# Kernel optimization log

Hardware: AMD Instinct MI355X
Metric: run time of the kernel (lower is better)

The kernel has to match this reference:

```python
import jax, jax.numpy as jnp
import numpy as np
from jax import lax

NUM_HEADS = 8
EPS = 1e-12  # torch F.normalize default eps


def setup_inputs() -> dict:
    key = jax.random.key(0)
    ks = jax.random.split(key, 7)
    B, C, H, W = 4, 128, 256, 256
    d = C // 2  # per-branch channels = 64
    x = jax.random.normal(ks[0], (B, C, H, W), jnp.float32)
    w_qkv1 = jax.random.normal(ks[1], (3 * d, d), jnp.float32) * 0.05
    w_qkv2 = jax.random.normal(ks[2], (3 * d, d), jnp.float32) * 0.05
    w_dw1 = jax.random.normal(ks[3], (3 * d, 1, 3, 3), jnp.float32) * 0.05
    w_dw2 = jax.random.normal(ks[4], (3 * d, 1, 3, 3), jnp.float32) * 0.05
    w_po1 = jax.random.normal(ks[5], (d, d), jnp.float32) * 0.05
    w_po2 = jax.random.normal(ks[6], (d, d), jnp.float32) * 0.05
    t1 = jnp.ones((NUM_HEADS, 1, 1), jnp.float32)
    t2 = jnp.ones((NUM_HEADS, 1, 1), jnp.float32)
    return {"x": x, "w_qkv1": w_qkv1, "w_qkv2": w_qkv2, "w_dw1": w_dw1,
            "w_dw2": w_dw2, "w_po1": w_po1, "w_po2": w_po2, "t1": t1, "t2": t2}


def _qkv(xb, w1x1, wdw):
    # 1x1 conv (pointwise) then 3x3 depthwise conv, no bias
    y = jnp.einsum('bchw,oc->bohw', xb, w1x1)
    y = lax.conv_general_dilated(
        y, wdw, window_strides=(1, 1), padding='SAME',
        dimension_numbers=('NCHW', 'OIHW', 'NCHW'),
        feature_group_count=y.shape[1])
    return y


def _heads(t, b, h, w):
    # b (head c) h w -> b head c (h*w)
    return t.reshape(b, NUM_HEADS, -1, h * w)


def _l2norm(t):
    n = jnp.sqrt(jnp.sum(t * t, axis=-1, keepdims=True))
    return t / jnp.maximum(n, EPS)


def reference(x, w_qkv1, w_qkv2, w_dw1, w_dw2, w_po1, w_po2, t1, t2):
    b, c, h, w = x.shape
    x1, x2 = jnp.split(x, 2, axis=1)
    q1, k1, v1 = jnp.split(_qkv(x1, w_qkv1, w_dw1), 3, axis=1)
    q2, k2, v2 = jnp.split(_qkv(x2, w_qkv2, w_dw2), 3, axis=1)
    q1, k1, v1 = (_heads(t, b, h, w) for t in (q1, k1, v1))
    q2, k2, v2 = (_heads(t, b, h, w) for t in (q2, k2, v2))
    q1, k1 = _l2norm(q1), _l2norm(k1)
    q2, k2 = _l2norm(q2), _l2norm(k2)
    # channel-wise attention: [b, head, c_h, c_h]
    attn1 = jax.nn.softmax(jnp.einsum('bhcn,bhdn->bhcd', q1, k1) * t1[None], axis=-1)
    attn2 = jax.nn.softmax(jnp.einsum('bhcn,bhdn->bhcd', q2, k2) * t2[None], axis=-1)
    # cross-branch V swap
    out1 = jnp.einsum('bhcd,bhdn->bhcn', attn1, v2).reshape(b, c // 2, h, w)
    out2 = jnp.einsum('bhcd,bhdn->bhcn', attn2, v1).reshape(b, c // 2, h, w)
    out1 = jnp.einsum('bchw,oc->bohw', out1, w_po1)
    out2 = jnp.einsum('bchw,oc->bohw', out2, w_po2)
    return jnp.concatenate([out1, out2], axis=1)
```

## Files before the change

kernel.cpp:

```cpp
#include <hip/hip_runtime.h>
#include <hip/hip_fp16.h>

#define NPIX 65536
#define WIMG 256
#define HIMG 256
#define TW 16
#define TH 8
#define HSTR 24
#define NSLOT 240
#define YCH 248

typedef __attribute__((ext_vector_type(8))) _Float16 half8;
typedef __attribute__((ext_vector_type(4))) float f32x4;

__device__ __forceinline__ unsigned int h2u(__half2 h) {
  union { __half2 h; unsigned int u; } c; c.h = h; return c.u;
}
__device__ __forceinline__ __half2 u2h(unsigned int u) {
  union { unsigned int u; __half2 h; } c; c.u = u; return c.h;
}
__device__ __forceinline__ __half2 sp2(_Float16 s) {
  union { _Float16 h[2]; __half2 v; } u; u.h[0] = s; u.h[1] = s; return u.v;
}
__device__ __forceinline__ int qk_idx(int ch, int pxblk) {
  return ch * 128 + ((pxblk ^ (ch & 7)) << 3);
}
__device__ __forceinline__ void ld16_lds(const void* g, void* l) {
  __builtin_amdgcn_global_load_lds(
      (const __attribute__((address_space(1))) unsigned int*)g,
      (__attribute__((address_space(3))) unsigned int*)l, 16, 0, 0);
}

__global__ void k_zero(float* __restrict__ p, int n) {
  int i = blockIdx.x * 256 + threadIdx.x;
  if (i < n) p[i] = 0.0f;
}

__global__ __launch_bounds__(256)
void k_wprep(const float* __restrict__ wq1, const float* __restrict__ wq2,
             const float* __restrict__ wd1, const float* __restrict__ wd2,
             _Float16* __restrict__ wqh, _Float16* __restrict__ wdh) {
  int i = blockIdx.x * 256 + threadIdx.x;
  if (i < 24576) {
    int br = i / 12288, j = i - br * 12288;
    wqh[i] = (_Float16)((br ? wq2 : wq1)[j]);
  } else if (i < 24576 + 6144) {
    int j = i - 24576;
    int br = j / 3072, r = j - br * 3072;
    int o = r >> 4, t = r & 15;
    wdh[j] = (t < 9) ? (_Float16)((br ? wd2 : wd1)[o * 9 + t]) : (_Float16)0.0f;
  }
}

__global__ __launch_bounds__(256)
void k_xt(const float* __restrict__ x, __half* __restrict__ xT) {
  __shared__ _Float16 tile[64 * 257];
  const int strip = blockIdx.x;
  const int br = blockIdx.y, b = blockIdx.z;
  const int tid = threadIdx.x;
  const float* xb = x + ((size_t)b * 128 + br * 64) * NPIX + strip * 256;
  #pragma unroll 8
  for (int c = 0; c < 64; ++c)
    tile[c * 257 + tid] = (_Float16)xb[(size_t)c * NPIX + tid];
  __syncthreads();
  __half* xo = xT + ((size_t)(b * 2 + br) * NPIX + strip * 256) * 64;
  const int j = tid & 7;
  #pragma unroll
  for (int i = 0; i < 8; ++i) {
    int p = (tid >> 3) + i * 32;
    half8 h;
    #pragma unroll
    for (int k = 0; k < 8; ++k) h[k] = tile[(j * 8 + k) * 257 + p];
    *(half8*)((_Float16*)xo + p * 64 + j * 8) = h;
  }
}

__global__ __launch_bounds__(256, 3)
void k_qkv(const __half* __restrict__ xT,
           const _Float16* __restrict__ wqh, const _Float16* __restrict__ wdh,
           const float* __restrict__ zpage,
           __half* __restrict__ vbuf, float* __restrict__ gram,
           float* __restrict__ sqq, float* __restrict__ sqk)
{
  __shared__ __align__(16) _Float16 xs[256 * 64];
  __shared__ __align__(16) _Float16 ys[2 * 16 * YCH];

  const int tid = threadIdx.x;
  const int lane = tid & 63;
  const int wid = tid >> 6;
  const int tile = blockIdx.x;
  const int br = blockIdx.y;
  const int b = blockIdx.z;
  const int tx0 = (tile & 15) * TW;
  const int ty0 = (tile >> 4) * TH;

  const _Float16* wqb = wqh + br * 12288;
  const _Float16* wdb = wdh + br * 3072;
  const __half* xTimg = xT + (size_t)(b * 2 + br) * NPIX * 64;

  {
    const int j = lane & 7, pl = lane >> 3;
    for (int it = wid; it < 30; it += 4) {
      int s = it * 8;
      int slot = s + pl;
      int hy = slot / HSTR;
      int hx = slot - hy * HSTR;
      int gy = ty0 - 1 + hy, gx = tx0 - 1 + hx;
      bool valid = (hx < 18) && ((unsigned)gy < HIMG) && ((unsigned)gx < WIMG);
      const void* src = valid
        ? (const void*)((const _Float16*)xTimg + (size_t)(gy * WIMG + gx) * 64
                        + ((j ^ (slot & 7)) << 3))
        : (const void*)((const char*)zpage + lane * 16);
      ld16_lds(src, (void*)(xs + s * 64));
    }
  }
  asm volatile("s_waitcnt vmcnt(0)" ::: "memory");
  __syncthreads();

  const int col = lane & 15;
  const int qrow = lane >> 4;
  const int rel = wid * 4 + (lane >> 4);
  const int row = (lane >> 1) & 7;
  const int half = lane & 1;

  unsigned int qreg[4][4], kreg[4][4];

#define PW16(S) do {                                                          \
    const int p_ = (S) >> 2, hh_ = (S) & 3;                                   \
    _Float16* yb_ = ys + ((S) & 1) * (16 * YCH);                              \
    const _Float16* wp_ = wqb + (((p_ * 64 + hh_ * 16 + col) << 6) + qrow * 8); \
    half8 wf0_ = *(const half8*)(wp_);                                        \
    half8 wf1_ = *(const half8*)(wp_ + 32);                                   \
    for (int mt = wid; mt < 15; mt += 4) {                                    \
      int px = mt * 16 + col;                                                 \
      half8 af0 = *(const half8*)(xs + px * 64 + (((qrow    ) ^ (px & 7)) << 3)); \
      half8 af1 = *(const half8*)(xs + px * 64 + (((4 + qrow) ^ (px & 7)) << 3)); \
      f32x4 a0 = {0,0,0,0};                                                   \
      a0 = __builtin_amdgcn_mfma_f32_16x16x32_f16(af0, wf0_, a0, 0, 0, 0);    \
      a0 = __builtin_amdgcn_mfma_f32_16x16x32_f16(af1, wf1_, a0, 0, 0, 0);    \
      int pxd = mt * 16 + qrow * 4;                                           \
      uint2 s0_ = {h2u(__floats2half2_rn(a0[0], a0[1])),                      \
                   h2u(__floats2half2_rn(a0[2], a0[3]))};                     \
      *(uint2*)(yb_ + col * YCH + pxd) = s0_;                                 \
    }                                                                         \
  } while (0)

#define DW16(S) do {                                                          \
    const int p_ = (S) >> 2, hh_ = (S) & 3;                                   \
    const _Float16* yb_ = ys + ((S) & 1) * (16 * YCH);                        \
    const int o_ = hh_ * 16 + rel;                                            \
    const _Float16* wdp_ = wdb + ((p_ * 64 + o_) << 4);                       \
    half8 wv_ = *(const half8*)wdp_;                                          \
    _Float16 w8_ = wdp_[8];                                                   \
    __half2 w2_[9];                                                           \
    _Pragma("unroll")                                                         \
    for (int j = 0; j < 8; ++j) w2_[j] = sp2(wv_[j]);                         \
    w2_[8] = sp2(w8_);                                                        \
    __half2 a_[4];                                                            \
    _Pragma("unroll")                                                         \
    for (int k2 = 0; k2 < 4; ++k2) a_[k2] = u2h(0u);                          \
    _Pragma("unroll")                                                         \
    for (int ky = 0; ky < 3; ++ky) {                                          \
      const _Float16* rp_ = yb_ + rel * YCH + (row + ky) * HSTR + half * 8;   \
      uint2 ra_ = *(const uint2*)rp_;                                         \
      uint2 rb_ = *(const uint2*)(rp_ + 4);                                   \
      unsigned int rc_ = *(const unsigned int*)(rp_ + 8);                     \
      unsigned int W_[5] = {ra_.x, ra_.y, rb_.x, rb_.y, rc_};                 \
      _Pragma("unroll")                                                       \
      for (int k2 = 0; k2 < 4; ++k2) {                                        \
        unsigned int M_ = (W_[k2] >> 16) | (W_[k2 + 1] << 16);                \
        a_[k2] = __hfma2(w2_[ky * 3 + 0], u2h(W_[k2]), a_[k2]);               \
        a_[k2] = __hfma2(w2_[ky * 3 + 1], u2h(M_), a_[k2]);                   \
        a_[k2] = __hfma2(w2_[ky * 3 + 2], u2h(W_[k2 + 1]), a_[k2]);           \
      }                                                                       \
    }                                                                         \
    if (p_ == 0) {                                                            \
      _Pragma("unroll")                                                       \
      for (int k2 = 0; k2 < 4; ++k2) qreg[hh_][k2] = h2u(a_[k2]);             \
    } else if (p_ == 1) {                                                     \
      _Pragma("unroll")                                                       \
      for (int k2 = 0; k2 < 4; ++k2) kreg[hh_][k2] = h2u(a_[k2]);             \
    } else {                                                                  \
      __half* vrow_ = (__half*)(vbuf                                          \
          + ((size_t)((br * 4 + b) * 64 + o_)) * NPIX                         \
          + (ty0 + row) * WIMG + tx0 + half * 8);                             \
      uint4 s_ = {h2u(a_[0]), h2u(a_[1]), h2u(a_[2]), h2u(a_[3])};            \
      *(uint4*)vrow_ = s_;                                                    \
    }                                                                         \
  } while (0)

  PW16(0);  __syncthreads();
  PW16(1);  DW16(0);  __syncthreads();
  PW16(2);  DW16(1);  __syncthreads();
  PW16(3);  DW16(2);  __syncthreads();
  PW16(4);  DW16(3);  __syncthreads();
  PW16(5);  DW16(4);  __syncthreads();
  PW16(6);  DW16(5);  __syncthreads();
  PW16(7);  DW16(6);  __syncthreads();
  PW16(8);  DW16(7);  __syncthreads();
  PW16(9);  DW16(8);  __syncthreads();
  PW16(10); DW16(9);  __syncthreads();
  PW16(11); DW16(10); __syncthreads();
  DW16(11);

  {
    _Float16* qsb = xs;
    _Float16* ksb = xs + 64 * 128;
    const int pb = row * 2 + half;
    #pragma unroll
    for (int hh = 0; hh < 4; ++hh) {
      int ch = hh * 16 + rel;
      uint4 q_ = {qreg[hh][0], qreg[hh][1], qreg[hh][2], qreg[hh][3]};
      uint4 k_ = {kreg[hh][0], kreg[hh][1], kreg[hh][2], kreg[hh][3]};
      *(uint4*)(qsb + qk_idx(ch, pb)) = q_;
      *(uint4*)(ksb + qk_idx(ch, pb)) = k_;
    }
  }
  __syncthreads();

  {
    const _Float16* qsb = xs;
    const _Float16* ksb = xs + 64 * 128;
    f32x4 gqk = {0,0,0,0}, gqq = {0,0,0,0}, gkk = {0,0,0,0};
    int ch = wid * 16 + col;
    #pragma unroll
    for (int kc = 0; kc < 4; ++kc) {
      int pb = kc * 4 + qrow;
      half8 aq = *(const half8*)(qsb + qk_idx(ch, pb));
      half8 bk = *(const half8*)(ksb + qk_idx(ch, pb));
      gqk = __builtin_amdgcn_mfma_f32_16x16x32_f16(aq, bk, gqk, 0, 0, 0);
      gqq = __builtin_amdgcn_mfma_f32_16x16x32_f16(aq, aq, gqq, 0, 0, 0);
      gkk = __builtin_amdgcn_mfma_f32_16x16x32_f16(bk, bk, gkk, 0, 0, 0);
    }
    const int gb_off = (br * 4 + b);
    if (((lane >> 3) & 1) == (lane >> 5)) {
      float* gb = gram + gb_off * 512;
      int kch = ch;
      int qc0 = wid * 16 + qrow * 4;
      #pragma unroll
      for (int r = 0; r < 4; ++r) {
        int qch = qc0 + r;
        atomicAdd(&gb[(qch >> 3) * 64 + (qch & 7) * 8 + (kch & 7)], gqk[r]);
      }
    }
    if ((col >> 2) == qrow) {
      atomicAdd(&sqq[gb_off * 64 + ch], gqq[lane & 3]);
      atomicAdd(&sqk[gb_off * 64 + ch], gkk[lane & 3]);
    }
  }
#undef PW16
#undef DW16
}

__global__ __launch_bounds__(64)
void k_attn(const float* __restrict__ gram, const float* __restrict__ sqq,
            const float* __restrict__ sqk,
            const float* __restrict__ wpo1, const float* __restrict__ wpo2,
            const float* __restrict__ t1, const float* __restrict__ t2,
            float* __restrict__ weff)
{
  const int br = blockIdx.x, b = blockIdx.y;
  const int t = threadIdx.x;
  __shared__ float attn[8][8][8];
  const float* gb = gram + (br * 4 + b) * 512;
  const float* sq = sqq + (br * 4 + b) * 64;
  const float* sk = sqk + (br * 4 + b) * 64;
  const float* tt = br ? t2 : t1;
  {
    int h = t >> 3, cq = t & 7;
    float ts = tt[h];
    float qn = fmaxf(sqrtf(sq[h * 8 + cq]), 1e-12f);
    float lg[8], m = -1e30f;
    #pragma unroll
    for (int d2 = 0; d2 < 8; ++d2) {
      float kn = fmaxf(sqrtf(sk[h * 8 + d2]), 1e-12f);
      lg[d2] = ts * gb[h * 64 + cq * 8 + d2] / (qn * kn);
      m = fmaxf(m, lg[d2]);
    }
    float s = 0.f;
    #pragma unroll
    for (int d2 = 0; d2 < 8; ++d2) { lg[d2] = expf(lg[d2] - m); s += lg[d2]; }
    float inv = 1.0f / s;
    #pragma unroll
    for (int d2 = 0; d2 < 8; ++d2) attn[h][cq][d2] = lg[d2] * inv;
  }
  __syncthreads();
  const float* wpo = br ? wpo2 : wpo1;
  float* wb = weff + (br * 4 + b) * 4096;
  for (int cp = 0; cp < 64; ++cp) {
    int hp = cp >> 3, ip = cp & 7;
    float acc = 0.f;
    #pragma unroll
    for (int j = 0; j < 8; ++j)
      acc += wpo[t * 64 + hp * 8 + j] * attn[hp][j][ip];
    wb[cp * 64 + t] = acc;
  }
}

__global__ __launch_bounds__(256)
void k_out(const __half* __restrict__ vbuf, const float* __restrict__ weff,
           float* __restrict__ out)
{
  const int obr = blockIdx.y, b = blockIdx.z;
  const int px = blockIdx.x * 256 + threadIdx.x;
  const float* wb = weff + (obr * 4 + b) * 4096;
  const __half* vp = vbuf + ((size_t)((1 - obr) * 4 + b) * 64) * NPIX + px;
  float acc[64];
  #pragma unroll
  for (int o = 0; o < 64; ++o) acc[o] = 0.0f;
  for (int c = 0; c < 64; ++c) {
    float vc = __half2float(vp[(size_t)c * NPIX]);
    const float* wr = wb + c * 64;
    #pragma unroll
    for (int o = 0; o < 64; ++o) acc[o] = fmaf(wr[o], vc, acc[o]);
  }
  float* op = out + ((size_t)b * 128 + obr * 64) * NPIX + px;
  #pragma unroll
  for (int o = 0; o < 64; ++o) op[(size_t)o * NPIX] = acc[o];
}

extern "C" void kernel_launch(void* const* d_in, const int* in_sizes, int n_in,
                              void* d_out, int out_size, void* d_ws, size_t ws_size,
                              hipStream_t stream) {
  const float* x     = (const float*)d_in[0];
  const float* wqkv1 = (const float*)d_in[1];
  const float* wqkv2 = (const float*)d_in[2];
  const float* wdw1  = (const float*)d_in[3];
  const float* wdw2  = (const float*)d_in[4];
  const float* wpo1  = (const float*)d_in[5];
  const float* wpo2  = (const float*)d_in[6];
  const float* t1    = (const float*)d_in[7];
  const float* t2    = (const float*)d_in[8];

  char* ws = (char*)d_ws;
  __half* vbuf = (__half*)ws;
  float* gram  = (float*)(ws + 67108864);
  float* sqq   = gram + 4096;
  float* sqk   = sqq + 512;
  float* zpage = sqk + 512;
  float* weff  = zpage + 1024;
  _Float16* wqkvh = (_Float16*)(weff + 32768);
  _Float16* wdwh  = wqkvh + 24576;

  __half* xT = (__half*)d_out;

  k_zero<<<dim3(24), dim3(256), 0, stream>>>(gram, 6144);
  k_wprep<<<dim3(120), dim3(256), 0, stream>>>(wqkv1, wqkv2, wdw1, wdw2, wqkvh, wdwh);
  k_xt<<<dim3(256, 2, 4), dim3(256), 0, stream>>>(x, xT);
  k_qkv<<<dim3(512, 2, 4), dim3(256), 0, stream>>>(xT, wqkvh, wdwh,
                                                   zpage, vbuf, gram, sqq, sqk);
  k_attn<<<dim3(2, 4), dim3(64), 0, stream>>>(gram, sqq, sqk, wpo1, wpo2, t1, t2, weff);
  k_out<<<dim3(256, 2, 4), dim3(256), 0, stream>>>(vbuf, weff, (float*)d_out);
}
```

Baseline: 254.3 us.

## Specialize warps: two waves do pointwise MFMA, two do depthwise conv

Splits the four waves of the fused QKV kernel into roles. Waves 0-1 run the pointwise MFMA for each stage while waves 2-3 run the depthwise 3x3 for the previous stage, each depthwise thread now covering two channels. The aim is to let the MFMA work and the VALU stencil work run at the same time on different waves, instead of every wave doing both in sequence. The cost is that each role does twice as much work per wave, and the depthwise waves hold twice as many q/k registers, which may raise register pressure.

```diff
diff --git a/kernel.cpp b/kernel.cpp
--- a/kernel.cpp
+++ b/kernel.cpp
@@ -119,11 +119,12 @@
 
   const int col = lane & 15;
   const int qrow = lane >> 4;
-  const int rel = wid * 4 + (lane >> 4);
-  const int row = (lane >> 1) & 7;
-  const int half = lane & 1;
-
-  unsigned int qreg[4][4], kreg[4][4];
+  const int idx  = tid & 127;
+  const int c0   = idx >> 4;
+  const int row  = (idx >> 1) & 7;
+  const int half = idx & 1;
+
+  unsigned int qreg[4][2][4], kreg[4][2][4];
 
 #define PW16(S) do {                                                          \
     const int p_ = (S) >> 2, hh_ = (S) & 3;                                   \
@@ -131,7 +132,7 @@
     const _Float16* wp_ = wqb + (((p_ * 64 + hh_ * 16 + col) << 6) + qrow * 8); \
     half8 wf0_ = *(const half8*)(wp_);                                        \
     half8 wf1_ = *(const half8*)(wp_ + 32);                                   \
-    for (int mt = wid; mt < 15; mt += 4) {                                    \
+    for (int mt = wid; mt < 15; mt += 2) {                                    \
       int px = mt * 16 + col;                                                 \
       half8 af0 = *(const half8*)(xs + px * 64 + (((qrow    ) ^ (px & 7)) << 3)); \
       half8 af1 = *(const half8*)(xs + px * 64 + (((4 + qrow) ^ (px & 7)) << 3)); \
@@ -145,10 +146,11 @@
     }                                                                         \
   } while (0)
 
-#define DW16(S) do {                                                          \
+#define DW1(S, CC, JJ) do {                                                   \
     const int p_ = (S) >> 2, hh_ = (S) & 3;                                   \
     const _Float16* yb_ = ys + ((S) & 1) * (16 * YCH);                        \
-    const int o_ = hh_ * 16 + rel;                                            \
+    const int c_ = (CC);                                                      \
+    const int o_ = hh_ * 16 + c_;                                             \
     const _Float16* wdp_ = wdb + ((p_ * 64 + o_) << 4);                       \
     half8 wv_ = *(const half8*)wdp_;                                          \
     _Float16 w8_ = wdp_[8];                                                   \
@@ -161,7 +163,7 @@
     for (int k2 = 0; k2 < 4; ++k2) a_[k2] = u2h(0u);                          \
     _Pragma("unroll")                                                         \
     for (int ky = 0; ky < 3; ++ky) {                                          \
-      const _Float16* rp_ = yb_ + rel * YCH + (row + ky) * HSTR + half * 8;   \
+      const _Float16* rp_ = yb_ + c_ * YCH + (row + ky) * HSTR + half * 8;    \
       uint2 ra_ = *(const uint2*)rp_;                                         \
       uint2 rb_ = *(const uint2*)(rp_ + 4);                                   \
       unsigned int rc_ = *(const unsigned int*)(rp_ + 8);                     \
@@ -176,10 +178,10 @@
     }                                                                         \
     if (p_ == 0) {                                                            \
       _Pragma("unroll")                                                       \
-      for (int k2 = 0; k2 < 4; ++k2) qreg[hh_][k2] = h2u(a_[k2]);             \
+      for (int k2 = 0; k2 < 4; ++k2) qreg[hh_][JJ][k2] = h2u(a_[k2]);         \
     } else if (p_ == 1) {                                                     \
       _Pragma("unroll")                                                       \
-      for (int k2 = 0; k2 < 4; ++k2) kreg[hh_][k2] = h2u(a_[k2]);             \
+      for (int k2 = 0; k2 < 4; ++k2) kreg[hh_][JJ][k2] = h2u(a_[k2]);         \
     } else {                                                                  \
       __half* vrow_ = (__half*)(vbuf                                          \
           + ((size_t)((br * 4 + b) * 64 + o_)) * NPIX                         \
@@ -189,31 +191,36 @@
     }                                                                         \
   } while (0)
 
-  PW16(0);  __syncthreads();
-  PW16(1);  DW16(0);  __syncthreads();
-  PW16(2);  DW16(1);  __syncthreads();
-  PW16(3);  DW16(2);  __syncthreads();
-  PW16(4);  DW16(3);  __syncthreads();
-  PW16(5);  DW16(4);  __syncthreads();
-  PW16(6);  DW16(5);  __syncthreads();
-  PW16(7);  DW16(6);  __syncthreads();
-  PW16(8);  DW16(7);  __syncthreads();
-  PW16(9);  DW16(8);  __syncthreads();
-  PW16(10); DW16(9);  __syncthreads();
-  PW16(11); DW16(10); __syncthreads();
-  DW16(11);
-
-  {
+#define DWPAIR(S) do { DW1(S, c0, 0); DW1(S, c0 + 8, 1); } while (0)
+
+  if (wid < 2) PW16(0);
+  __syncthreads();
+  if (wid < 2) PW16(1);  else DWPAIR(0);   __syncthreads();
+  if (wid < 2) PW16(2);  else DWPAIR(1);   __syncthreads();
+  if (wid < 2) PW16(3);  else DWPAIR(2);   __syncthreads();
+  if (wid < 2) PW16(4);  else DWPAIR(3);   __syncthreads();
+  if (wid < 2) PW16(5);  else DWPAIR(4);   __syncthreads();
+  if (wid < 2) PW16(6);  else DWPAIR(5);   __syncthreads();
+  if (wid < 2) PW16(7);  else DWPAIR(6);   __syncthreads();
+  if (wid < 2) PW16(8);  else DWPAIR(7);   __syncthreads();
+  if (wid < 2) PW16(9);  else DWPAIR(8);   __syncthreads();
+  if (wid < 2) PW16(10); else DWPAIR(9);   __syncthreads();
+  if (wid < 2) PW16(11); else DWPAIR(10);  __syncthreads();
+  if (wid >= 2) {
+    DWPAIR(11);
     _Float16* qsb = xs;
     _Float16* ksb = xs + 64 * 128;
     const int pb = row * 2 + half;
     #pragma unroll
-    for (int hh = 0; hh < 4; ++hh) {
-      int ch = hh * 16 + rel;
-      uint4 q_ = {qreg[hh][0], qreg[hh][1], qreg[hh][2], qreg[hh][3]};
-      uint4 k_ = {kreg[hh][0], kreg[hh][1], kreg[hh][2], kreg[hh][3]};
-      *(uint4*)(qsb + qk_idx(ch, pb)) = q_;
-      *(uint4*)(ksb + qk_idx(ch, pb)) = k_;
+    for (int g = 0; g < 4; ++g) {
+      #pragma unroll
+      for (int j = 0; j < 2; ++j) {
+        int ch = g * 16 + c0 + j * 8;
+        uint4 q_ = {qreg[g][j][0], qreg[g][j][1], qreg[g][j][2], qreg[g][j][3]};
+        uint4 k_ = {kreg[g][j][0], kreg[g][j][1], kreg[g][j][2], kreg[g][j][3]};
+        *(uint4*)(qsb + qk_idx(ch, pb)) = q_;
+        *(uint4*)(ksb + qk_idx(ch, pb)) = k_;
+      }
     }
   }
   __syncthreads();
@@ -249,7 +256,8 @@
     }
   }
 #undef PW16
-#undef DW16
+#undef DW1
+#undef DWPAIR
 }
 
 __global__ __launch_bounds__(64)
```

After: 264.6 us. 4.1% more time.
